# Performance work log

Hardware: AMD Instinct MI355X
Metric: run time of the kernel (lower is better)

The kernel has to match this reference:

```python
import jax, jax.numpy as jnp
import numpy as np

EMB = 1024
HEADS = 16
HEAD_DIM = EMB // HEADS
EPS = 1e-5


def setup_inputs() -> dict:
    key = jax.random.key(0)
    ks = jax.random.split(key, 10)
    B, T, D = 2, 2048, EMB
    s = 1.0 / np.sqrt(D)
    inp = {
        "x": jax.random.normal(ks[0], (B, T, D), dtype=jnp.float32),
        "wq": jax.random.normal(ks[1], (D, D), dtype=jnp.float32) * s,
        "bq": jnp.zeros((D,), jnp.float32),
        "wk": jax.random.normal(ks[2], (D, D), dtype=jnp.float32) * s,
        "bk": jnp.zeros((D,), jnp.float32),
        "wv": jax.random.normal(ks[3], (D, D), dtype=jnp.float32) * s,
        "bv": jnp.zeros((D,), jnp.float32),
        "wo": jax.random.normal(ks[4], (D, D), dtype=jnp.float32) * s,
        "bo": jnp.zeros((D,), jnp.float32),
        "gamma": jnp.ones((D,), jnp.float32),
        "beta": jnp.zeros((D,), jnp.float32),
    }
    return inp


def _attention(x, wq, bq, wk, bk, wv, bv, wo, bo, gamma, beta):
    B, T, D = x.shape
    H, Hd = HEADS, HEAD_DIM
    q = (x @ wq + bq).reshape(B, T, H, Hd)
    k = (x @ wk + bk).reshape(B, T, H, Hd)
    v = (x @ wv + bv).reshape(B, T, H, Hd)
    # scores: [B, H, T, T]
    scores = jnp.einsum("bthd,bshd->bhts", q, k) / np.sqrt(Hd)
    attn = jax.nn.softmax(scores, axis=-1)  # dropout is identity in eval
    ctx = jnp.einsum("bhts,bshd->bthd", attn, v).reshape(B, T, D)
    out = ctx @ wo + bo
    y = x + out  # residual (dropout identity)
    mu = jnp.mean(y, axis=-1, keepdims=True)
    var = jnp.var(y, axis=-1, keepdims=True)
    return (y - mu) * jax.lax.rsqrt(var + EPS) * gamma + beta


def reference(x, wq, bq, wk, bk, wv, bv, wo, bo, gamma, beta):
    return _attention(x, wq, bq, wk, bk, wv, bv, wo, bo, gamma, beta)
```

## Files before the change

### kernel.cpp

```cpp
#include <hip/hip_runtime.h>

#define BSZ   2
#define TSEQ  2048
#define DMOD  1024
#define NHEAD 16
#define HDIM  64
#define MROW  (BSZ*TSEQ)
#define LNEPS 1e-5f
#define QSCALE 0.18033688011f

typedef __bf16 bf16x8 __attribute__((ext_vector_type(8)));
typedef float  f32x4  __attribute__((ext_vector_type(4)));
typedef unsigned short us8 __attribute__((ext_vector_type(8)));
typedef unsigned short us4 __attribute__((ext_vector_type(4)));

__device__ __forceinline__ unsigned short f2bf(float f) {
    unsigned u = __float_as_uint(f);
    u += 0x7FFF + ((u >> 16) & 1);
    return (unsigned short)(u >> 16);
}
__device__ __forceinline__ float bf2f(unsigned short u) {
    return __uint_as_float((unsigned)u << 16);
}

__device__ __forceinline__ float fexp2(float x) {
#if __has_builtin(__builtin_amdgcn_exp2f)
    return __builtin_amdgcn_exp2f(x);
#else
    return __expf(x * 0.6931471805599453f);
#endif
}

__device__ __forceinline__ void gld_lds16(const void* g, void* l) {
    __builtin_amdgcn_global_load_lds(
        (const __attribute__((address_space(1))) unsigned int*)g,
        (__attribute__((address_space(3))) unsigned int*)l, 16, 0, 0);
}

__global__ __launch_bounds__(256) void prep_k(
    const float* __restrict__ x,
    const float* __restrict__ wq, const float* __restrict__ wk,
    const float* __restrict__ wv, const float* __restrict__ wo,
    unsigned short* __restrict__ Xb,
    unsigned short* __restrict__ WqkvT, unsigned short* __restrict__ WoT)
{
    const int tid = threadIdx.x;
    if (blockIdx.x < 2048) {
        const size_t i = ((size_t)blockIdx.x * 256 + tid) * 8;
        float4 a = *(const float4*)&x[i];
        float4 b = *(const float4*)&x[i + 4];
        union { unsigned short u[8]; uint4 v; } o;
        o.u[0]=f2bf(a.x); o.u[1]=f2bf(a.y); o.u[2]=f2bf(a.z); o.u[3]=f2bf(a.w);
        o.u[4]=f2bf(b.x); o.u[5]=f2bf(b.y); o.u[6]=f2bf(b.z); o.u[7]=f2bf(b.w);
        *(uint4*)&Xb[i] = o.v;
        return;
    }
    __shared__ float T[64][68];
    const int id = blockIdx.x - 2048;
    const int z  = id >> 8;
    const int bx = id & 15;
    const int by = (id >> 4) & 15;
    const float* W = (z == 0) ? wq : (z == 1) ? wk : (z == 2) ? wv : wo;
    unsigned short* Wt = (z < 3) ? (WqkvT + (size_t)z*1024*1024) : WoT;
    const int lr = tid >> 4, lc = (tid & 15) * 4;
    #pragma unroll
    for (int p = 0; p < 4; ++p) {
        const int kk = p*16 + lr;
        float4 v = *(const float4*)&W[(size_t)(by*64 + kk)*1024 + bx*64 + lc];
        T[lc+0][kk] = v.x; T[lc+1][kk] = v.y; T[lc+2][kk] = v.z; T[lc+3][kk] = v.w;
    }
    __syncthreads();
    #pragma unroll
    for (int p = 0; p < 2; ++p) {
        const int nl = p*32 + (tid >> 3);
        const int kb = (tid & 7) * 8;
        float4 a = *(const float4*)&T[nl][kb];
        float4 b = *(const float4*)&T[nl][kb+4];
        union { unsigned short u[8]; uint4 v; } o;
        o.u[0]=f2bf(a.x); o.u[1]=f2bf(a.y); o.u[2]=f2bf(a.z); o.u[3]=f2bf(a.w);
        o.u[4]=f2bf(b.x); o.u[5]=f2bf(b.y); o.u[6]=f2bf(b.z); o.u[7]=f2bf(b.w);
        *(uint4*)&Wt[(size_t)(bx*64 + nl)*1024 + by*64 + kb] = o.v;
    }
}


#define PH_SYNC() do { __builtin_amdgcn_s_barrier(); \
    asm volatile("s_waitcnt lgkmcnt(0)" ::: "memory"); \
    __builtin_amdgcn_sched_barrier(0); } while (0)

struct Core8 {
    const unsigned short *sA, *sB;
    unsigned short *A0w, *A1w, *B0w, *B1w;
    const unsigned short *fA0, *fA1, *fB0, *fB1;
    int swz0, swz1;
};

__device__ __forceinline__ void stage2(const unsigned short* s, unsigned short* d) {
    gld_lds16(s, d);
    gld_lds16(s + 64*1024, d + 4096);
}

__device__ __forceinline__ void core_setup(Core8& C, unsigned short* LDS,
    const unsigned short* A, const unsigned short* Bt, int bm, int bn, int kbase)
{
    const int tid = threadIdx.x;
    const int w = tid >> 6, lane = tid & 63;
    const int quad = lane >> 4, l16 = lane & 15;
    const int wm = w >> 2, wn = w & 3;
    const int r_l = lane >> 3, c_l = lane & 7;
    C.sA = A  + (size_t)(bm + w*8 + r_l)*1024 + (c_l ^ r_l)*8 + kbase;
    C.sB = Bt + (size_t)(bn + w*8 + r_l)*1024 + (c_l ^ r_l)*8 + kbase;
    unsigned short* A0 = LDS;
    unsigned short* A1 = LDS + 16384;
    unsigned short* B0 = LDS + 32768;
    unsigned short* B1 = LDS + 49152;
    C.A0w = A0 + w*512; C.A1w = A1 + w*512;
    C.B0w = B0 + w*512; C.B1w = B1 + w*512;
    C.fA0 = A0 + (wm*128 + l16)*64; C.fA1 = A1 + (wm*128 + l16)*64;
    C.fB0 = B0 + (wn*64 + l16)*64;  C.fB1 = B1 + (wn*64 + l16)*64;
    C.swz0 = ( quad      ^ (l16 & 7)) * 8;
    C.swz1 = ((4 + quad) ^ (l16 & 7)) * 8;
}

__device__ __forceinline__ void ld_b(const Core8& C, bf16x8 (&bfr)[4][2],
                                     const unsigned short* fB) {
    #pragma unroll
    for (int n = 0; n < 4; ++n) {
        bfr[n][0] = *(const bf16x8*)(fB + n*1024 + C.swz0);
        bfr[n][1] = *(const bf16x8*)(fB + n*1024 + C.swz1);
    }
}

template<int Q>
__device__ __forceinline__ void ld_a(const Core8& C, bf16x8 (&af)[2][2],
                                     const unsigned short* fA) {
    #pragma unroll
    for (int dm = 0; dm < 2; ++dm) {
        af[dm][0] = *(const bf16x8*)(fA + (Q*2+dm)*1024 + C.swz0);
        af[dm][1] = *(const bf16x8*)(fA + (Q*2+dm)*1024 + C.swz1);
    }
}

template<int Q>
__device__ __forceinline__ void mma_q(f32x4 (&acc)[8][4], bf16x8 (&af)[2][2],
                                      bf16x8 (&bfr)[4][2]) {
    __builtin_amdgcn_s_setprio(1);
    #pragma unroll
    for (int dm = 0; dm < 2; ++dm)
        #pragma unroll
        for (int n = 0; n < 4; ++n) {
            f32x4 t = acc[Q*2+dm][n];
            t = __builtin_amdgcn_mfma_f32_16x16x32_bf16(af[dm][0], bfr[n][0], t, 0, 0, 0);
            t = __builtin_amdgcn_mfma_f32_16x16x32_bf16(af[dm][1], bfr[n][1], t, 0, 0, 0);
            acc[Q*2+dm][n] = t;
        }
    __builtin_amdgcn_s_setprio(0);
}

template<int NIT>
__device__ __forceinline__ void core_kloop(const Core8& C, f32x4 (&acc)[8][4])
{
    stage2(C.sA,                 C.A0w);
    stage2(C.sA + 128*1024,      C.A0w + 8192);
    stage2(C.sB,                 C.B0w);
    stage2(C.sB + 128*1024,      C.B0w + 8192);
    stage2(C.sB + 64,            C.B1w);
    stage2(C.sB + 128*1024 + 64, C.B1w + 8192);
    asm volatile("s_waitcnt vmcnt(4)" ::: "memory");
    __builtin_amdgcn_s_barrier();

    bf16x8 bfr[4][2];
    bf16x8 af[2][2];

    #pragma unroll 1
    for (int it = 0; it < NIT - 1; ++it) {
        const int kk = it * 128;
        ld_b(C, bfr, C.fB0);
        ld_a<0>(C, af, C.fA0);
        stage2(C.sA + kk + 64,            C.A1w);
        stage2(C.sA + 128*1024 + kk + 64, C.A1w + 8192);
        PH_SYNC();  mma_q<0>(acc, af, bfr);
        __builtin_amdgcn_s_barrier();
        ld_a<1>(C, af, C.fA0);
        stage2(C.sB + kk + 128, C.B0w);
        PH_SYNC();  mma_q<1>(acc, af, bfr);
        __builtin_amdgcn_s_barrier();
        ld_a<2>(C, af, C.fA0);
        stage2(C.sB + 128*1024 + kk + 128, C.B0w + 8192);
        PH_SYNC();  mma_q<2>(acc, af, bfr);
        __builtin_amdgcn_s_barrier();
        ld_a<3>(C, af, C.fA0);
        PH_SYNC();  mma_q<3>(acc, af, bfr);
        asm volatile("s_waitcnt vmcnt(4)" ::: "memory");
        __builtin_amdgcn_s_barrier();
        ld_b(C, bfr, C.fB1);
        ld_a<0>(C, af, C.fA1);
        stage2(C.sA + kk + 128,            C.A0w);
        stage2(C.sA + 128*1024 + kk + 128, C.A0w + 8192);
        PH_SYNC();  mma_q<0>(acc, af, bfr);
        __builtin_amdgcn_s_barrier();
        ld_a<1>(C, af, C.fA1);
        stage2(C.sB + kk + 192, C.B1w);
        PH_SYNC();  mma_q<1>(acc, af, bfr);
        __builtin_amdgcn_s_barrier();
        ld_a<2>(C, af, C.fA1);
        stage2(C.sB + 128*1024 + kk + 192, C.B1w + 8192);
        PH_SYNC();  mma_q<2>(acc, af, bfr);
        __builtin_amdgcn_s_barrier();
        ld_a<3>(C, af, C.fA1);
        PH_SYNC();  mma_q<3>(acc, af, bfr);
        asm volatile("s_waitcnt vmcnt(4)" ::: "memory");
        __builtin_amdgcn_s_barrier();
    }

    {
        const int kk = (NIT - 1) * 128;
        ld_b(C, bfr, C.fB0);
        ld_a<0>(C, af, C.fA0);
        stage2(C.sA + kk + 64,            C.A1w);
        stage2(C.sA + 128*1024 + kk + 64, C.A1w + 8192);
        PH_SYNC();  mma_q<0>(acc, af, bfr);
        __builtin_amdgcn_s_barrier();
        ld_a<1>(C, af, C.fA0); PH_SYNC(); mma_q<1>(acc, af, bfr); __builtin_amdgcn_s_barrier();
        ld_a<2>(C, af, C.fA0); PH_SYNC(); mma_q<2>(acc, af, bfr); __builtin_amdgcn_s_barrier();
        ld_a<3>(C, af, C.fA0); PH_SYNC(); mma_q<3>(acc, af, bfr);
        asm volatile("s_waitcnt vmcnt(0)" ::: "memory");
        __builtin_amdgcn_s_barrier();
        ld_b(C, bfr, C.fB1);
        ld_a<0>(C, af, C.fA1); PH_SYNC(); mma_q<0>(acc, af, bfr); __builtin_amdgcn_s_barrier();
        ld_a<1>(C, af, C.fA1); PH_SYNC(); mma_q<1>(acc, af, bfr); __builtin_amdgcn_s_barrier();
        ld_a<2>(C, af, C.fA1); PH_SYNC(); mma_q<2>(acc, af, bfr); __builtin_amdgcn_s_barrier();
        ld_a<3>(C, af, C.fA1); PH_SYNC(); mma_q<3>(acc, af, bfr);
    }
}

__global__ __launch_bounds__(512, 2) void gemm_qkv_k(
    const unsigned short* __restrict__ A, const unsigned short* __restrict__ Bt,
    const float* __restrict__ b0, const float* __restrict__ b1,
    const float* __restrict__ b2,
    unsigned short* __restrict__ oQ, unsigned short* __restrict__ oK,
    unsigned short* __restrict__ oV)
{
    extern __shared__ unsigned short LDS[];
    const int ob = blockIdx.x;
    const int wg = (ob & 7) * 24 + (ob >> 3);
    const int by = wg / 12, bx = wg - by*12;
    const int bm = by * 256, bn = bx * 256;

    Core8 C;
    core_setup(C, LDS, A, Bt, bm, bn, 0);

    f32x4 acc[8][4];
    #pragma unroll
    for (int i = 0; i < 8; ++i)
        #pragma unroll
        for (int j = 0; j < 4; ++j) acc[i][j] = (f32x4){0.f,0.f,0.f,0.f};

    core_kloop<8>(C, acc);

    const int tid = threadIdx.x;
    const int w = tid >> 6, lane = tid & 63;
    const int quad = lane >> 4, l16 = lane & 15;
    const int wm = w >> 2, wn = w & 3;
    const int seg = bn >> 10;
    const int cb  = bn & 1023;
    if (seg < 2) {
        unsigned short* O = (seg == 0) ? oQ : oK;
        const float sc = (seg == 0) ? QSCALE : 1.0f;
        const float* bias = (seg == 0) ? b0 : b1;
        #pragma unroll
        for (int n = 0; n < 4; ++n) {
            const int col = cb + wn*64 + n*16 + l16;
            const float bs = bias[col];
            #pragma unroll
            for (int m = 0; m < 8; ++m)
                #pragma unroll
                for (int r = 0; r < 4; ++r) {
                    const int grow = bm + wm*128 + m*16 + quad*4 + r;
                    O[(size_t)grow*1024 + col] = f2bf((acc[m][n][r] + bs) * sc);
                }
        }
    } else {
        #pragma unroll
        for (int n = 0; n < 4; ++n) {
            const int ch = cb + wn*64 + n*16 + l16;
            const float bs = b2[ch];
            #pragma unroll
            for (int m = 0; m < 8; ++m) {
                const int grow0 = bm + wm*128 + m*16 + quad*4;
                us4 o;
                #pragma unroll
                for (int r = 0; r < 4; ++r) o[r] = f2bf(acc[m][n][r] + bs);
                *(us4*)&oV[(size_t)ch*MROW + grow0] = o;
            }
        }
    }
}

__global__ __launch_bounds__(512, 2) void gemm_proj_k(
    const unsigned short* __restrict__ A, const unsigned short* __restrict__ Bt,
    unsigned short* __restrict__ P)
{
    extern __shared__ unsigned short LDS[];
    const int ob = blockIdx.x;
    const int wg = (ob & 7) * 8 + (ob >> 3);
    const int by = wg >> 2, bx = wg & 3;
    const int kz = blockIdx.y;
    const int bm = by * 256, bn = bx * 256;

    Core8 C;
    core_setup(C, LDS, A, Bt, bm, bn, kz * 512);

    f32x4 acc[8][4];
    #pragma unroll
    for (int i = 0; i < 8; ++i)
        #pragma unroll
        for (int j = 0; j < 4; ++j) acc[i][j] = (f32x4){0.f,0.f,0.f,0.f};

    core_kloop<4>(C, acc);

    const int tid = threadIdx.x;
    const int w = tid >> 6, lane = tid & 63;
    const int quad = lane >> 4, l16 = lane & 15;
    const int wm = w >> 2, wn = w & 3;
    unsigned short* O = P + (size_t)kz*MROW*1024;
    #pragma unroll
    for (int n = 0; n < 4; ++n) {
        const int col = bn + wn*64 + n*16 + l16;
        #pragma unroll
        for (int m = 0; m < 8; ++m)
            #pragma unroll
            for (int r = 0; r < 4; ++r) {
                const int grow = bm + wm*128 + m*16 + quad*4 + r;
                O[(size_t)grow*1024 + col] = f2bf(acc[m][n][r]);
            }
    }
}

__global__ __launch_bounds__(256, 2) void attn_k(
    const unsigned short* __restrict__ Qg,
    const unsigned short* __restrict__ Kg,
    const unsigned short* __restrict__ Vtg,
    unsigned short* __restrict__ CTX)
{
    __shared__ __align__(16) char lds_raw[51200];
    unsigned short* Qs = (unsigned short*)lds_raw;
    unsigned short* Ks = (unsigned short*)(lds_raw + 18432);
    unsigned short* Vs = (unsigned short*)(lds_raw + 34816);
    float* Od = (float*)lds_raw;
    float* Ld = (float*)(lds_raw + 34816);

    const int tid  = threadIdx.x;
    const int wv   = tid >> 6;
    const int lane = tid & 63;
    const int quad = lane >> 4;
    const int l16  = lane & 15;
    const int wq   = wv & 1;
    const int wk   = wv >> 1;
    const int qb   = blockIdx.x * 128;
    const int h    = blockIdx.y;
    const int b    = blockIdx.z;

    {
        const int row = tid & 127, cb = (tid >> 7) * 32;
        const unsigned short* Qrow = Qg + ((size_t)(b*TSEQ + qb + row))*DMOD + h*HDIM + cb;
        #pragma unroll
        for (int j = 0; j < 4; ++j)
            *(us8*)&Qs[row*72 + cb + j*8] = *(const us8*)&Qrow[j*8];
    }
    __syncthreads();
    bf16x8 qf[4][2];
    #pragma unroll
    for (int nt = 0; nt < 4; ++nt)
        #pragma unroll
        for (int kh = 0; kh < 2; ++kh)
            qf[nt][kh] = *(const bf16x8*)&Qs[(wq*64 + nt*16 + l16)*72 + kh*32 + quad*8];

    const int sr = lane >> 3;
    const int sc = lane & 7;
    const bool isK = (wv < 2);
    const int half = wv & 1;
    const unsigned short* gbase;
    unsigned int goff[8];
    unsigned short* ldst;
    if (isK) {
        gbase = Kg + ((size_t)(b*TSEQ + half*1024))*DMOD + h*HDIM;
        #pragma unroll
        for (int s = 0; s < 8; ++s) {
            const int R = s*8 + sr;
            const int gc = sc ^ ((R ^ (R >> 2)) & 7);
            goff[s] = (unsigned)(R*DMOD + gc*8);
        }
        ldst = Ks + half*4096;
    } else {
        gbase = Vtg + ((size_t)(h*HDIM))*MROW + b*TSEQ + half*1024;
        #pragma unroll
        for (int s = 0; s < 8; ++s) {
            const int D = s*8 + sr;
            const int gc = sc ^ (D & 7);
            goff[s] = (unsigned)(D*MROW + gc*8);
        }
        ldst = Vs + half*4096;
    }
    const size_t gstep = isK ? (size_t)64*DMOD : (size_t)64;

    const int rowA_l = (l16 >> 2)*8 + (l16 & 3);
    const int rowB_l = rowA_l + 4;
    const int swA = (rowA_l ^ (rowA_l >> 2)) & 7;
    const int swB = (rowB_l ^ (rowB_l >> 2)) & 7;
    const unsigned short* KsW = Ks + wk*4096;
    const unsigned short* VsW = Vs + wk*4096;

    bf16x8 onef;
    { union { unsigned short u[8]; bf16x8 v; } o1;
      #pragma unroll
      for (int i = 0; i < 8; ++i) o1.u[i] = 0x3F80;
      onef = o1.v; }

    f32x4 oacc[4][4];
    f32x4 lacc[4];
    #pragma unroll
    for (int dt = 0; dt < 4; ++dt)
        #pragma unroll
        for (int nt = 0; nt < 4; ++nt) oacc[dt][nt] = (f32x4){0.f,0.f,0.f,0.f};
    #pragma unroll
    for (int nt = 0; nt < 4; ++nt) lacc[nt] = (f32x4){0.f,0.f,0.f,0.f};

    for (int it = 0; it < 16; ++it) {
        __syncthreads();
        #pragma unroll
        for (int s = 0; s < 8; ++s)
            gld_lds16(gbase + (size_t)it*gstep + goff[s], ldst + s*512);
        __syncthreads();

        #pragma unroll
        for (int gl = 0; gl < 2; ++gl) {
            const int rA = gl*32 + rowA_l;
            const int rB = gl*32 + rowB_l;
            bf16x8 ka0 = *(const bf16x8*)&KsW[rA*64 + ((quad     ^ swA))*8];
            bf16x8 ka1 = *(const bf16x8*)&KsW[rA*64 + (((4+quad) ^ swA))*8];
            bf16x8 kb0 = *(const bf16x8*)&KsW[rB*64 + ((quad     ^ swB))*8];
            bf16x8 kb1 = *(const bf16x8*)&KsW[rB*64 + (((4+quad) ^ swB))*8];
            bf16x8 vf[4];
            #pragma unroll
            for (int dt = 0; dt < 4; ++dt)
                vf[dt] = *(const bf16x8*)&VsW[(dt*16 + l16)*64 + ((gl*4 + quad) ^ (l16 & 7))*8];

            #pragma unroll
            for (int nt = 0; nt < 4; ++nt) {
                f32x4 z = (f32x4){0.f,0.f,0.f,0.f};
                z = __builtin_amdgcn_mfma_f32_16x16x32_bf16(ka0, qf[nt][0], z, 0, 0, 0);
                f32x4 sA = __builtin_amdgcn_mfma_f32_16x16x32_bf16(ka1, qf[nt][1], z, 0, 0, 0);
                z = (f32x4){0.f,0.f,0.f,0.f};
                z = __builtin_amdgcn_mfma_f32_16x16x32_bf16(kb0, qf[nt][0], z, 0, 0, 0);
                f32x4 sB = __builtin_amdgcn_mfma_f32_16x16x32_bf16(kb1, qf[nt][1], z, 0, 0, 0);

                float eA[4], eB[4];
                #pragma unroll
                for (int r = 0; r < 4; ++r) { eA[r] = fexp2(sA[r]); eB[r] = fexp2(sB[r]); }
                union { unsigned d[4]; bf16x8 v; } up;
                up.d[0] = __builtin_amdgcn_perm(__float_as_uint(eA[1]), __float_as_uint(eA[0]), 0x07060302);
                up.d[1] = __builtin_amdgcn_perm(__float_as_uint(eA[3]), __float_as_uint(eA[2]), 0x07060302);
                up.d[2] = __builtin_amdgcn_perm(__float_as_uint(eB[1]), __float_as_uint(eB[0]), 0x07060302);
                up.d[3] = __builtin_amdgcn_perm(__float_as_uint(eB[3]), __float_as_uint(eB[2]), 0x07060302);
                const bf16x8 pf = up.v;

                lacc[nt] = __builtin_amdgcn_mfma_f32_16x16x32_bf16(onef, pf, lacc[nt], 0, 0, 0);
                #pragma unroll
                for (int dt = 0; dt < 4; ++dt)
                    oacc[dt][nt] = __builtin_amdgcn_mfma_f32_16x16x32_bf16(vf[dt], pf, oacc[dt][nt], 0, 0, 0);
            }
        }
    }

    __syncthreads();
    if (wk == 0) {
        float* od = Od + wq*64*68;
        #pragma unroll
        for (int nt = 0; nt < 4; ++nt) {
            #pragma unroll
            for (int dt = 0; dt < 4; ++dt)
                *(f32x4*)&od[(nt*16 + l16)*68 + dt*16 + quad*4] = oacc[dt][nt];
            if (quad == 0) Ld[wq*64 + nt*16 + l16] = lacc[nt][0];
        }
    }
    __syncthreads();
    if (wk == 1) {
        const float* od = Od + wq*64*68;
        #pragma unroll
        for (int nt = 0; nt < 4; ++nt) {
            const float l = Ld[wq*64 + nt*16 + l16] + lacc[nt][0];
            const float inv = 1.f / l;
            const int q = qb + wq*64 + nt*16 + l16;
            unsigned short* crow = CTX + ((size_t)(b*TSEQ + q))*DMOD + h*HDIM;
            #pragma unroll
            for (int dt = 0; dt < 4; ++dt) {
                f32x4 p = *(const f32x4*)&od[(nt*16 + l16)*68 + dt*16 + quad*4];
                us4 o;
                #pragma unroll
                for (int r = 0; r < 4; ++r) o[r] = f2bf((p[r] + oacc[dt][nt][r]) * inv);
                *(us4*)&crow[dt*16 + quad*4] = o;
            }
        }
    }
}

__global__ __launch_bounds__(256) void red_ln_k(
    const float* __restrict__ x, const unsigned short* __restrict__ P,
    const float* __restrict__ bo,
    const float* __restrict__ gamma, const float* __restrict__ beta,
    float* __restrict__ out)
{
    __shared__ float rs[4], rss[4];
    const int row = blockIdx.x;
    const int tid = threadIdx.x;
    const int c = tid * 4;
    const float4 xv = *(const float4*)&x[(size_t)row*DMOD + c];
    const us4 p0 = *(const us4*)&P[(size_t)row*DMOD + c];
    const us4 p1 = *(const us4*)&P[(size_t)(MROW + row)*DMOD + c];
    const float4 bv4 = *(const float4*)&bo[c];
    const float v0 = xv.x + bf2f(p0[0]) + bf2f(p1[0]) + bv4.x;
    const float v1 = xv.y + bf2f(p0[1]) + bf2f(p1[1]) + bv4.y;
    const float v2 = xv.z + bf2f(p0[2]) + bf2f(p1[2]) + bv4.z;
    const float v3 = xv.w + bf2f(p0[3]) + bf2f(p1[3]) + bv4.w;
    float s  = v0 + v1 + v2 + v3;
    float ss = v0*v0 + v1*v1 + v2*v2 + v3*v3;
    #pragma unroll
    for (int o = 32; o > 0; o >>= 1) {
        s  += __shfl_down(s,  o, 64);
        ss += __shfl_down(ss, o, 64);
    }
    if ((tid & 63) == 0) { rs[tid >> 6] = s; rss[tid >> 6] = ss; }
    __syncthreads();
    s  = rs[0] + rs[1] + rs[2] + rs[3];
    ss = rss[0] + rss[1] + rss[2] + rss[3];
    const float mean = s * (1.f/DMOD);
    const float var  = ss * (1.f/DMOD) - mean*mean;
    const float rstd = rsqrtf(var + LNEPS);
    const float4 gv = *(const float4*)&gamma[c];
    const float4 bv = *(const float4*)&beta[c];
    float4 o;
    o.x = (v0 - mean)*rstd*gv.x + bv.x;
    o.y = (v1 - mean)*rstd*gv.y + bv.y;
    o.z = (v2 - mean)*rstd*gv.z + bv.z;
    o.w = (v3 - mean)*rstd*gv.w + bv.w;
    *(float4*)&out[(size_t)row*DMOD + c] = o;
}

extern "C" void kernel_launch(void* const* d_in, const int* in_sizes, int n_in,
                              void* d_out, int out_size, void* d_ws, size_t ws_size,
                              hipStream_t stream) {
    const float* x     = (const float*)d_in[0];
    const float* wq    = (const float*)d_in[1];
    const float* bq    = (const float*)d_in[2];
    const float* wk    = (const float*)d_in[3];
    const float* bk    = (const float*)d_in[4];
    const float* wvp   = (const float*)d_in[5];
    const float* bvp   = (const float*)d_in[6];
    const float* wo    = (const float*)d_in[7];
    const float* bo    = (const float*)d_in[8];
    const float* gamma = (const float*)d_in[9];
    const float* beta  = (const float*)d_in[10];
    float* out = (float*)d_out;

    unsigned short* Xb    = (unsigned short*)d_ws;
    unsigned short* WqkvT = Xb    + (size_t)MROW*DMOD;
    unsigned short* WoT   = WqkvT + (size_t)3072*1024;
    unsigned short* Qb    = WoT   + (size_t)1024*1024;
    unsigned short* Kb    = Qb    + (size_t)MROW*DMOD;
    unsigned short* VtG   = Kb    + (size_t)MROW*DMOD;
    unsigned short* CTXb  = VtG   + (size_t)DMOD*MROW;
    unsigned short* Pp    = Qb;

    prep_k<<<3072, 256, 0, stream>>>(x, wq, wk, wvp, wo, Xb, WqkvT, WoT);

    gemm_qkv_k<<<dim3(192), 512, 131072, stream>>>(
        Xb, WqkvT, bq, bk, bvp, Qb, Kb, VtG);

    attn_k<<<dim3(TSEQ/128, NHEAD, BSZ), 256, 0, stream>>>(Qb, Kb, VtG, CTXb);

    gemm_proj_k<<<dim3(64, 2), 512, 131072, stream>>>(CTXb, WoT, Pp);

    red_ln_k<<<MROW, 256, 0, stream>>>(x, Pp, bo, gamma, beta, out);
}
```

Baseline: 194.2 us.

## Double-buffer attention K/V tiles and split projection GEMM four ways over K

The attention kernel now uses 64KB of dynamic LDS holding two K/V buffers. It prefetches the next tile with direct global-to-LDS loads while computing on the current one, which removes one barrier per iteration. MFMA sections are bracketed with s_setprio so matrix work gets issue priority. The output projection GEMM is split into four K-slices instead of two to raise the block count, and the LayerNorm reduction sums four partials from a separate workspace buffer. The costs are higher LDS use per block, which may lower occupancy, and extra partial-sum traffic.

```diff
diff --git a/kernel.cpp b/kernel.cpp
--- a/kernel.cpp
+++ b/kernel.cpp
@@ -309,7 +309,7 @@
     const int bm = by * 256, bn = bx * 256;
 
     Core8 C;
-    core_setup(C, LDS, A, Bt, bm, bn, kz * 512);
+    core_setup(C, LDS, A, Bt, bm, bn, kz * 256);
 
     f32x4 acc[8][4];
     #pragma unroll
@@ -317,7 +317,7 @@
         #pragma unroll
         for (int j = 0; j < 4; ++j) acc[i][j] = (f32x4){0.f,0.f,0.f,0.f};
 
-    core_kloop<4>(C, acc);
+    core_kloop<2>(C, acc);
 
     const int tid = threadIdx.x;
     const int w = tid >> 6, lane = tid & 63;
@@ -343,12 +343,11 @@
     const unsigned short* __restrict__ Vtg,
     unsigned short* __restrict__ CTX)
 {
-    __shared__ __align__(16) char lds_raw[51200];
+    extern __shared__ __align__(16) char lds_raw[];
+    unsigned short* KV = (unsigned short*)lds_raw;
     unsigned short* Qs = (unsigned short*)lds_raw;
-    unsigned short* Ks = (unsigned short*)(lds_raw + 18432);
-    unsigned short* Vs = (unsigned short*)(lds_raw + 34816);
     float* Od = (float*)lds_raw;
-    float* Ld = (float*)(lds_raw + 34816);
+    float* Ld = (float*)(lds_raw + 65536);
 
     const int tid  = threadIdx.x;
     const int wv   = tid >> 6;
@@ -375,6 +374,7 @@
         #pragma unroll
         for (int kh = 0; kh < 2; ++kh)
             qf[nt][kh] = *(const bf16x8*)&Qs[(wq*64 + nt*16 + l16)*72 + kh*32 + quad*8];
+    __syncthreads();
 
     const int sr = lane >> 3;
     const int sc = lane & 7;
@@ -382,7 +382,7 @@
     const int half = wv & 1;
     const unsigned short* gbase;
     unsigned int goff[8];
-    unsigned short* ldst;
+    unsigned short* ldstb;
     if (isK) {
         gbase = Kg + ((size_t)(b*TSEQ + half*1024))*DMOD + h*HDIM;
         #pragma unroll
@@ -391,7 +391,7 @@
             const int gc = sc ^ ((R ^ (R >> 2)) & 7);
             goff[s] = (unsigned)(R*DMOD + gc*8);
         }
-        ldst = Ks + half*4096;
+        ldstb = KV + half*4096;
     } else {
         gbase = Vtg + ((size_t)(h*HDIM))*MROW + b*TSEQ + half*1024;
         #pragma unroll
@@ -400,7 +400,7 @@
             const int gc = sc ^ (D & 7);
             goff[s] = (unsigned)(D*MROW + gc*8);
         }
-        ldst = Vs + half*4096;
+        ldstb = KV + 16384 + half*4096;
     }
     const size_t gstep = isK ? (size_t)64*DMOD : (size_t)64;
 
@@ -408,8 +408,6 @@
     const int rowB_l = rowA_l + 4;
     const int swA = (rowA_l ^ (rowA_l >> 2)) & 7;
     const int swB = (rowB_l ^ (rowB_l >> 2)) & 7;
-    const unsigned short* KsW = Ks + wk*4096;
-    const unsigned short* VsW = Vs + wk*4096;
 
     bf16x8 onef;
     { union { unsigned short u[8]; bf16x8 v; } o1;
@@ -426,12 +424,23 @@
     #pragma unroll
     for (int nt = 0; nt < 4; ++nt) lacc[nt] = (f32x4){0.f,0.f,0.f,0.f};
 
+    #pragma unroll
+    for (int s = 0; s < 8; ++s)
+        gld_lds16(gbase + goff[s], ldstb + s*512);
+    __syncthreads();
+
     for (int it = 0; it < 16; ++it) {
-        __syncthreads();
-        #pragma unroll
-        for (int s = 0; s < 8; ++s)
-            gld_lds16(gbase + (size_t)it*gstep + goff[s], ldst + s*512);
-        __syncthreads();
+        const int cbuf = (it & 1) * 8192;
+        if (it < 15) {
+            const unsigned short* gn = gbase + (size_t)(it+1)*gstep;
+            unsigned short* d = ldstb + (cbuf ^ 8192);
+            #pragma unroll
+            for (int s = 0; s < 8; ++s)
+                gld_lds16(gn + goff[s], d + s*512);
+        }
+        __builtin_amdgcn_sched_barrier(0);
+        const unsigned short* KsW = KV + cbuf + wk*4096;
+        const unsigned short* VsW = KV + 16384 + cbuf + wk*4096;
 
         #pragma unroll
         for (int gl = 0; gl < 2; ++gl) {
@@ -448,12 +457,14 @@
 
             #pragma unroll
             for (int nt = 0; nt < 4; ++nt) {
+                __builtin_amdgcn_s_setprio(1);
                 f32x4 z = (f32x4){0.f,0.f,0.f,0.f};
                 z = __builtin_amdgcn_mfma_f32_16x16x32_bf16(ka0, qf[nt][0], z, 0, 0, 0);
                 f32x4 sA = __builtin_amdgcn_mfma_f32_16x16x32_bf16(ka1, qf[nt][1], z, 0, 0, 0);
                 z = (f32x4){0.f,0.f,0.f,0.f};
                 z = __builtin_amdgcn_mfma_f32_16x16x32_bf16(kb0, qf[nt][0], z, 0, 0, 0);
                 f32x4 sB = __builtin_amdgcn_mfma_f32_16x16x32_bf16(kb1, qf[nt][1], z, 0, 0, 0);
+                __builtin_amdgcn_s_setprio(0);
 
                 float eA[4], eB[4];
                 #pragma unroll
@@ -465,15 +476,17 @@
                 up.d[3] = __builtin_amdgcn_perm(__float_as_uint(eB[3]), __float_as_uint(eB[2]), 0x07060302);
                 const bf16x8 pf = up.v;
 
+                __builtin_amdgcn_s_setprio(1);
                 lacc[nt] = __builtin_amdgcn_mfma_f32_16x16x32_bf16(onef, pf, lacc[nt], 0, 0, 0);
                 #pragma unroll
                 for (int dt = 0; dt < 4; ++dt)
                     oacc[dt][nt] = __builtin_amdgcn_mfma_f32_16x16x32_bf16(vf[dt], pf, oacc[dt][nt], 0, 0, 0);
+                __builtin_amdgcn_s_setprio(0);
             }
         }
-    }
-
-    __syncthreads();
+        __syncthreads();
+    }
+
     if (wk == 0) {
         float* od = Od + wq*64*68;
         #pragma unroll
@@ -518,11 +531,13 @@
     const float4 xv = *(const float4*)&x[(size_t)row*DMOD + c];
     const us4 p0 = *(const us4*)&P[(size_t)row*DMOD + c];
     const us4 p1 = *(const us4*)&P[(size_t)(MROW + row)*DMOD + c];
+    const us4 p2 = *(const us4*)&P[(size_t)(2*MROW + row)*DMOD + c];
+    const us4 p3 = *(const us4*)&P[(size_t)(3*MROW + row)*DMOD + c];
     const float4 bv4 = *(const float4*)&bo[c];
-    const float v0 = xv.x + bf2f(p0[0]) + bf2f(p1[0]) + bv4.x;
-    const float v1 = xv.y + bf2f(p0[1]) + bf2f(p1[1]) + bv4.y;
-    const float v2 = xv.z + bf2f(p0[2]) + bf2f(p1[2]) + bv4.z;
-    const float v3 = xv.w + bf2f(p0[3]) + bf2f(p1[3]) + bv4.w;
+    const float v0 = xv.x + bf2f(p0[0]) + bf2f(p1[0]) + bf2f(p2[0]) + bf2f(p3[0]) + bv4.x;
+    const float v1 = xv.y + bf2f(p0[1]) + bf2f(p1[1]) + bf2f(p2[1]) + bf2f(p3[1]) + bv4.y;
+    const float v2 = xv.z + bf2f(p0[2]) + bf2f(p1[2]) + bf2f(p2[2]) + bf2f(p3[2]) + bv4.z;
+    const float v3 = xv.w + bf2f(p0[3]) + bf2f(p1[3]) + bf2f(p2[3]) + bf2f(p3[3]) + bv4.w;
     float s  = v0 + v1 + v2 + v3;
     float ss = v0*v0 + v1*v1 + v2*v2 + v3*v3;
     #pragma unroll
@@ -570,16 +585,16 @@
     unsigned short* Kb    = Qb    + (size_t)MROW*DMOD;
     unsigned short* VtG   = Kb    + (size_t)MROW*DMOD;
     unsigned short* CTXb  = VtG   + (size_t)DMOD*MROW;
-    unsigned short* Pp    = Qb;
+    unsigned short* Pp    = CTXb  + (size_t)MROW*DMOD;
 
     prep_k<<<3072, 256, 0, stream>>>(x, wq, wk, wvp, wo, Xb, WqkvT, WoT);
 
     gemm_qkv_k<<<dim3(192), 512, 131072, stream>>>(
         Xb, WqkvT, bq, bk, bvp, Qb, Kb, VtG);
 
-    attn_k<<<dim3(TSEQ/128, NHEAD, BSZ), 256, 0, stream>>>(Qb, Kb, VtG, CTXb);
-
-    gemm_proj_k<<<dim3(64, 2), 512, 131072, stream>>>(CTXb, WoT, Pp);
+    attn_k<<<dim3(TSEQ/128, NHEAD, BSZ), 256, 66048, stream>>>(Qb, Kb, VtG, CTXb);
+
+    gemm_proj_k<<<dim3(64, 4), 512, 131072, stream>>>(CTXb, WoT, Pp);
 
     red_ln_k<<<MROW, 256, 0, stream>>>(x, Pp, bo, gamma, beta, out);
 }
```

Result: no change. 191.9 us (-1.2%).
